# Performance work log

Hardware: AMD Instinct MI355X
Metric: run time of the kernel (lower is better)

The kernel has to match this reference:

```python
import math
import jax, jax.numpy as jnp
import numpy as np

ALPHA = 0.2  # LeakyReLU negative slope
MASK_VAL = -9e15


def _positional_encoding(n: int, d: int) -> jnp.ndarray:
    # Custom PE with a (1 + exp(-pos/100)) decay factor, matching CustomPositionalEncoding
    position = jnp.arange(n, dtype=jnp.float32)[:, None]            # [N,1]
    div_term = jnp.exp(jnp.arange(0, d, 2, dtype=jnp.float32) * (-math.log(10000.0) / d))
    decay = 1.0 + jnp.exp(-position / 100.0)                         # [N,1]
    pe = jnp.zeros((n, d), dtype=jnp.float32)
    pe = pe.at[:, 0::2].set(jnp.sin(position * div_term) * decay)
    pe = pe.at[:, 1::2].set(jnp.cos(position * div_term) * decay)
    return pe[None]                                                  # [1,N,d]


def setup_inputs() -> dict:
    key = jax.random.key(0)
    k_h, k_adj, k_W, k_a = jax.random.split(key, 4)
    B, N, IN_F, OUT_F = 8, 2048, 128, 128
    h = jax.random.normal(k_h, (B, N, IN_F), dtype=jnp.float32)
    # sparse-ish 0/1 adjacency (float, as in the torch module)
    adj = jax.random.randint(k_adj, (B, N, N), 0, 2).astype(jnp.float32)
    # xavier_uniform init scale
    limW = math.sqrt(6.0 / (IN_F + OUT_F))
    W = jax.random.uniform(k_W, (IN_F, OUT_F), minval=-limW, maxval=limW, dtype=jnp.float32)
    lima = math.sqrt(6.0 / (2 * OUT_F + 1))
    a = jax.random.uniform(k_a, (2 * OUT_F, 1), minval=-lima, maxval=lima, dtype=jnp.float32)
    return {"h": h, "adj": adj, "W": W, "a": a}


def reference(h, adj, W, a):
    B, N, _ = h.shape
    out_f = W.shape[1]
    h = h + _positional_encoding(N, h.shape[2])
    # force self-loops
    eye = jnp.eye(N, dtype=adj.dtype)[None]
    adj = jnp.where(eye > 0, jnp.ones_like(adj), adj)
    Wh = jnp.einsum('bni,io->bno', h, W)                 # [B,N,out_f]
    a1 = a[:out_f, 0]
    a2 = a[out_f:, 0]
    s1 = Wh @ a1                                          # [B,N]
    s2 = Wh @ a2                                          # [B,N]
    e = s1[:, :, None] + s2[:, None, :]                   # [B,N,N] additive score
    e = jnp.where(e >= 0, e, ALPHA * e)                   # leaky relu
    attn = jnp.where(adj > 0, e, MASK_VAL)
    attn = jax.nn.softmax(attn, axis=-1)
    # dropout is identity in eval mode
    h_prime = jnp.einsum('bnm,bmo->bno', attn, Wh)        # [B,N,out_f]
    deg = adj.sum(-1)                                     # [B,N]
    valid = deg > 0
    valid = valid.at[:, 0].set(False)
    denom = jnp.clip(valid.sum(1, keepdims=True), 1, None).astype(h_prime.dtype)  # [B,1]
    g = (h_prime * valid[:, :, None]).sum(1) / denom      # [B,out_f] masked mean pool
    return jax.nn.elu(g)
```

## Files before the change

kernel.cpp:

```cpp
#include <hip/hip_runtime.h>
#include <math.h>

#define NN 2048
#define BATCH 8
#define FDIM 128
#define MASKV -9000000000000000.0f
#define LALPHA 0.2f

__global__ void k_zero(float* __restrict__ c, float* __restrict__ gpre) {
    int i = blockIdx.x * 256 + threadIdx.x;
    if (i < BATCH * NN) c[i] = 0.f;
    if (i < BATCH * FDIM) gpre[i] = 0.f;
}

__global__ void k_pe(float* __restrict__ pe) {
    int i = blockIdx.x * 256 + threadIdx.x;
    int n = i >> 7;
    int k = i & 127;
    int jj = k >> 1;
    float dt = expf((float)(2 * jj) * (-0.07195578415606394f));
    float ang = (float)n * dt;
    float decay = 1.f + expf(-(float)n * 0.01f);
    float v = ((k & 1) == 0 ? sinf(ang) : cosf(ang)) * decay;
    pe[i] = v;
}

__global__ __launch_bounds__(256) void k_wh(const float* __restrict__ h,
                                            const float* __restrict__ pe,
                                            const float* __restrict__ W,
                                            const float* __restrict__ a,
                                            float* __restrict__ Wh,
                                            float* __restrict__ s1,
                                            float* __restrict__ s2) {
    __shared__ float w_lds[64 * 128];
    __shared__ float hpe_lds[64 * 68];
    const int b  = blockIdx.y;
    const int n0 = blockIdx.x * 64;
    const int t  = threadIdx.x;
    const int tc = t & 15;
    const int tr = t >> 4;

    float acc[4][8];
#pragma unroll
    for (int i = 0; i < 4; i++)
#pragma unroll
        for (int j = 0; j < 8; j++) acc[i][j] = 0.f;

    for (int kp = 0; kp < 2; ++kp) {
        {
            const float4* wsrc = (const float4*)(W + kp * 64 * 128);
            float4* wdst = (float4*)w_lds;
#pragma unroll
            for (int q = 0; q < 8; q++) wdst[t + q * 256] = wsrc[t + q * 256];
        }
        {
#pragma unroll
            for (int q = 0; q < 4; q++) {
                int f = t + q * 256;
                int r = f >> 4;
                int k4 = (f & 15) << 2;
                int n = n0 + r;
                int kk = kp * 64 + k4;
                const float* hp_src = h + ((size_t)b * NN + n) * FDIM + kk;
                float4 hv = *(const float4*)hp_src;
                float4 pv = *(const float4*)(pe + (size_t)n * FDIM + kk);
                float4 hpv = make_float4(hv.x + pv.x, hv.y + pv.y,
                                         hv.z + pv.z, hv.w + pv.w);
                *(float4*)(hpe_lds + r * 68 + k4) = hpv;
            }
        }
        __syncthreads();
#pragma unroll 4
        for (int k = 0; k < 64; k++) {
            float wv[8];
            float4 wa = *(float4*)(w_lds + k * 128 + tc * 8);
            float4 wb = *(float4*)(w_lds + k * 128 + tc * 8 + 4);
            wv[0] = wa.x; wv[1] = wa.y; wv[2] = wa.z; wv[3] = wa.w;
            wv[4] = wb.x; wv[5] = wb.y; wv[6] = wb.z; wv[7] = wb.w;
#pragma unroll
            for (int i = 0; i < 4; i++) {
                float hv = hpe_lds[(tr * 4 + i) * 68 + k];
#pragma unroll
                for (int j = 0; j < 8; j++) acc[i][j] = fmaf(hv, wv[j], acc[i][j]);
            }
        }
        __syncthreads();
    }

    float a1v[8], a2v[8];
#pragma unroll
    for (int j = 0; j < 8; j++) { a1v[j] = a[tc * 8 + j]; a2v[j] = a[FDIM + tc * 8 + j]; }
#pragma unroll
    for (int i = 0; i < 4; i++) {
        int n = n0 + tr * 4 + i;
        float* dst = Wh + ((size_t)b * NN + n) * FDIM + tc * 8;
        *(float4*)dst = make_float4(acc[i][0], acc[i][1], acc[i][2], acc[i][3]);
        *(float4*)(dst + 4) = make_float4(acc[i][4], acc[i][5], acc[i][6], acc[i][7]);
        float p1 = 0.f, p2 = 0.f;
#pragma unroll
        for (int j = 0; j < 8; j++) {
            p1 = fmaf(acc[i][j], a1v[j], p1);
            p2 = fmaf(acc[i][j], a2v[j], p2);
        }
#pragma unroll
        for (int off = 1; off < 16; off <<= 1) {
            p1 += __shfl_xor(p1, off, 64);
            p2 += __shfl_xor(p2, off, 64);
        }
        if (tc == 0) {
            s1[(size_t)b * NN + n] = p1;
            s2[(size_t)b * NN + n] = p2;
        }
    }
}

__global__ __launch_bounds__(256) void k_attn(const float* __restrict__ adj,
                                              const float* __restrict__ s1,
                                              const float* __restrict__ s2,
                                              float* __restrict__ c) {
    const int b = blockIdx.y;
    const int chunk = blockIdx.x;
    const int t = threadIdx.x;
    const int wave = t >> 6;
    const int lane = t & 63;
    __shared__ float c_lds[NN];
    for (int i = t; i < NN; i += 256) c_lds[i] = 0.f;

    const float* s2b = s2 + (size_t)b * NN;
    float s2v[32];
#pragma unroll
    for (int kq = 0; kq < 8; kq++) {
        float4 v = *(const float4*)(s2b + kq * 256 + lane * 4);
        s2v[kq * 4 + 0] = v.x; s2v[kq * 4 + 1] = v.y;
        s2v[kq * 4 + 2] = v.z; s2v[kq * 4 + 3] = v.w;
    }
    float c_acc[32];
#pragma unroll
    for (int j = 0; j < 32; j++) c_acc[j] = 0.f;

    const int nbase = chunk * 32;
    const float* adjb = adj + (size_t)b * NN * NN;
    const float* s1b = s1 + (size_t)b * NN;

    for (int r = wave; r < 32; r += 4) {
        int n = nbase + r;
        if (n == 0) continue;
        float s1n = s1b[n];
        const float* arow = adjb + (size_t)n * NN;
        float val[32];
        float vmax = MASKV;
#pragma unroll
        for (int kq = 0; kq < 8; kq++) {
            float4 av = *(const float4*)(arow + kq * 256 + lane * 4);
            float a4[4] = {av.x, av.y, av.z, av.w};
#pragma unroll
            for (int e = 0; e < 4; e++) {
                int m = kq * 256 + lane * 4 + e;
                float ev = s1n + s2v[kq * 4 + e];
                ev = (ev >= 0.f) ? ev : LALPHA * ev;
                bool conn = (a4[e] > 0.f) || (m == n);
                float v = conn ? ev : MASKV;
                val[kq * 4 + e] = v;
                vmax = fmaxf(vmax, v);
            }
        }
#pragma unroll
        for (int off = 32; off; off >>= 1) vmax = fmaxf(vmax, __shfl_xor(vmax, off, 64));
        float zsum = 0.f;
#pragma unroll
        for (int j = 0; j < 32; j++) {
            float p = __expf(val[j] - vmax);
            val[j] = p;
            zsum += p;
        }
#pragma unroll
        for (int off = 32; off; off >>= 1) zsum += __shfl_xor(zsum, off, 64);
        float rz = 1.f / zsum;
#pragma unroll
        for (int j = 0; j < 32; j++) c_acc[j] = fmaf(val[j], rz, c_acc[j]);
    }

    __syncthreads();
    for (int w = 0; w < 4; w++) {
        if (wave == w) {
#pragma unroll
            for (int kq = 0; kq < 8; kq++)
#pragma unroll
                for (int e = 0; e < 4; e++)
                    c_lds[kq * 256 + lane * 4 + e] += c_acc[kq * 4 + e];
        }
        __syncthreads();
    }
    for (int i = t; i < NN; i += 256)
        atomicAdd(&c[(size_t)b * NN + i], c_lds[i]);
}

__global__ __launch_bounds__(256) void k_gpre(const float* __restrict__ Wh,
                                              const float* __restrict__ c,
                                              float* __restrict__ gpre) {
    const int b = blockIdx.y;
    const int m0 = blockIdx.x * 64;
    const int t = threadIdx.x;
    const int o = t & 127;
    const int mh = t >> 7;
    __shared__ float c_lds[64];
    if (t < 64) c_lds[t] = c[(size_t)b * NN + m0 + t];
    __syncthreads();
    float acc = 0.f;
    const float* whb = Wh + ((size_t)b * NN + m0 + mh * 32) * FDIM;
#pragma unroll 4
    for (int mm = 0; mm < 32; mm++)
        acc = fmaf(c_lds[mh * 32 + mm], whb[mm * FDIM + o], acc);
    atomicAdd(&gpre[b * FDIM + o], acc);
}

__global__ void k_elu(const float* __restrict__ gpre, float* __restrict__ out) {
    int i = blockIdx.x * 256 + threadIdx.x;
    if (i < BATCH * FDIM) {
        float g = gpre[i] * (1.0f / 2047.0f);
        out[i] = g > 0.f ? g : expm1f(g);
    }
}

extern "C" void kernel_launch(void* const* d_in, const int* in_sizes, int n_in,
                              void* d_out, int out_size, void* d_ws, size_t ws_size,
                              hipStream_t stream) {
    (void)in_sizes; (void)n_in; (void)out_size; (void)ws_size;
    const float* h   = (const float*)d_in[0];
    const float* adj = (const float*)d_in[1];
    const float* W   = (const float*)d_in[2];
    const float* a   = (const float*)d_in[3];
    float* out = (float*)d_out;

    char* ws = (char*)d_ws;
    float* Wh   = (float*)ws;
    float* pe   = (float*)(ws + (size_t)BATCH * NN * FDIM * 4);
    float* s1   = pe + (size_t)NN * FDIM;
    float* s2   = s1 + (size_t)BATCH * NN;
    float* c    = s2 + (size_t)BATCH * NN;
    float* gpre = c + (size_t)BATCH * NN;

    hipLaunchKernelGGL(k_zero, dim3(64), dim3(256), 0, stream, c, gpre);
    hipLaunchKernelGGL(k_pe, dim3(NN * FDIM / 256), dim3(256), 0, stream, pe);
    hipLaunchKernelGGL(k_wh, dim3(NN / 64, BATCH), dim3(256), 0, stream,
                       h, pe, W, a, Wh, s1, s2);
    hipLaunchKernelGGL(k_attn, dim3(NN / 32, BATCH), dim3(256), 0, stream,
                       adj, s1, s2, c);
    hipLaunchKernelGGL(k_gpre, dim3(NN / 64, BATCH), dim3(256), 0, stream,
                       Wh, c, gpre);
    hipLaunchKernelGGL(k_elu, dim3(4), dim3(256), 0, stream, gpre, out);
}
```

Baseline: 223.4 us.

## Replace atomic column-sum accumulation with partial buffers and deterministic reductions

The attention kernel now processes 16 rows per block (doubling the grid). Each wave writes its column-sum partial to its own LDS slice, the slices are summed in one pass, and the block writes a per-chunk partial row instead of issuing global atomics. The pooling and ELU kernels then reduce these partial buffers, which removes the zeroing kernel and all atomics. The cost is extra workspace traffic (an 8x128x2048 partial buffer, about 8 MB, read back in the pooling kernel) and a 64-way serial sum in the final kernel.

```diff
diff --git a/kernel.cpp b/kernel.cpp
--- a/kernel.cpp
+++ b/kernel.cpp
@@ -5,13 +5,6 @@
 #define BATCH 8
 #define FDIM 128
 #define MASKV -9000000000000000.0f
-#define LALPHA 0.2f
-
-__global__ void k_zero(float* __restrict__ c, float* __restrict__ gpre) {
-    int i = blockIdx.x * 256 + threadIdx.x;
-    if (i < BATCH * NN) c[i] = 0.f;
-    if (i < BATCH * FDIM) gpre[i] = 0.f;
-}
 
 __global__ void k_pe(float* __restrict__ pe) {
     int i = blockIdx.x * 256 + threadIdx.x;
@@ -117,14 +110,13 @@
 __global__ __launch_bounds__(256) void k_attn(const float* __restrict__ adj,
                                               const float* __restrict__ s1,
                                               const float* __restrict__ s2,
-                                              float* __restrict__ c) {
+                                              float* __restrict__ c_part) {
     const int b = blockIdx.y;
     const int chunk = blockIdx.x;
     const int t = threadIdx.x;
     const int wave = t >> 6;
     const int lane = t & 63;
-    __shared__ float c_lds[NN];
-    for (int i = t; i < NN; i += 256) c_lds[i] = 0.f;
+    __shared__ float c_lds[4][NN];
 
     const float* s2b = s2 + (size_t)b * NN;
     float s2v[32];
@@ -138,12 +130,13 @@
 #pragma unroll
     for (int j = 0; j < 32; j++) c_acc[j] = 0.f;
 
-    const int nbase = chunk * 32;
+    const int nbase = chunk * 16;
     const float* adjb = adj + (size_t)b * NN * NN;
     const float* s1b = s1 + (size_t)b * NN;
 
-    for (int r = wave; r < 32; r += 4) {
-        int n = nbase + r;
+#pragma unroll 1
+    for (int ri = 0; ri < 4; ri++) {
+        int n = nbase + wave * 4 + ri;
         if (n == 0) continue;
         float s1n = s1b[n];
         const float* arow = adjb + (size_t)n * NN;
@@ -156,8 +149,8 @@
 #pragma unroll
             for (int e = 0; e < 4; e++) {
                 int m = kq * 256 + lane * 4 + e;
-                float ev = s1n + s2v[kq * 4 + e];
-                ev = (ev >= 0.f) ? ev : LALPHA * ev;
+                float x = s1n + s2v[kq * 4 + e];
+                float ev = fmaxf(x, 0.2f * x);
                 bool conn = (a4[e] > 0.f) || (m == n);
                 float v = conn ? ev : MASKV;
                 val[kq * 4 + e] = v;
@@ -180,44 +173,67 @@
         for (int j = 0; j < 32; j++) c_acc[j] = fmaf(val[j], rz, c_acc[j]);
     }
 
+#pragma unroll
+    for (int kq = 0; kq < 8; kq++)
+        *(float4*)(&c_lds[wave][kq * 256 + lane * 4]) =
+            make_float4(c_acc[kq * 4 + 0], c_acc[kq * 4 + 1],
+                        c_acc[kq * 4 + 2], c_acc[kq * 4 + 3]);
     __syncthreads();
-    for (int w = 0; w < 4; w++) {
-        if (wave == w) {
-#pragma unroll
-            for (int kq = 0; kq < 8; kq++)
-#pragma unroll
-                for (int e = 0; e < 4; e++)
-                    c_lds[kq * 256 + lane * 4 + e] += c_acc[kq * 4 + e];
-        }
-        __syncthreads();
-    }
-    for (int i = t; i < NN; i += 256)
-        atomicAdd(&c[(size_t)b * NN + i], c_lds[i]);
+    float* dst = c_part + ((size_t)b * 128 + chunk) * NN;
+#pragma unroll
+    for (int q = 0; q < 2; q++) {
+        int idx = t + q * 256;
+        float4 v0 = ((float4*)c_lds[0])[idx];
+        float4 v1 = ((float4*)c_lds[1])[idx];
+        float4 v2 = ((float4*)c_lds[2])[idx];
+        float4 v3 = ((float4*)c_lds[3])[idx];
+        ((float4*)dst)[idx] = make_float4(v0.x + v1.x + v2.x + v3.x,
+                                          v0.y + v1.y + v2.y + v3.y,
+                                          v0.z + v1.z + v2.z + v3.z,
+                                          v0.w + v1.w + v2.w + v3.w);
+    }
 }
 
 __global__ __launch_bounds__(256) void k_gpre(const float* __restrict__ Wh,
-                                              const float* __restrict__ c,
-                                              float* __restrict__ gpre) {
+                                              const float* __restrict__ c_part,
+                                              float* __restrict__ g_part) {
     const int b = blockIdx.y;
-    const int m0 = blockIdx.x * 64;
+    const int mc = blockIdx.x;
+    const int m0 = mc * 64;
     const int t = threadIdx.x;
+    __shared__ float red[256];
+    __shared__ float c_lds[64];
+
+    {
+        const int mi = t & 63;
+        const int w = t >> 6;
+        const float* cp = c_part + (size_t)b * 128 * NN + m0 + mi;
+        float s = 0.f;
+#pragma unroll 8
+        for (int j = 0; j < 32; j++) s += cp[(size_t)(w * 32 + j) * NN];
+        red[w * 64 + mi] = s;
+    }
+    __syncthreads();
+    if (t < 64) c_lds[t] = red[t] + red[t + 64] + red[t + 128] + red[t + 192];
+    __syncthreads();
+
     const int o = t & 127;
     const int mh = t >> 7;
-    __shared__ float c_lds[64];
-    if (t < 64) c_lds[t] = c[(size_t)b * NN + m0 + t];
-    __syncthreads();
     float acc = 0.f;
     const float* whb = Wh + ((size_t)b * NN + m0 + mh * 32) * FDIM;
 #pragma unroll 4
     for (int mm = 0; mm < 32; mm++)
         acc = fmaf(c_lds[mh * 32 + mm], whb[mm * FDIM + o], acc);
-    atomicAdd(&gpre[b * FDIM + o], acc);
-}
-
-__global__ void k_elu(const float* __restrict__ gpre, float* __restrict__ out) {
+    g_part[((size_t)(mc * 2 + mh)) * (BATCH * FDIM) + b * FDIM + o] = acc;
+}
+
+__global__ void k_elu(const float* __restrict__ g_part, float* __restrict__ out) {
     int i = blockIdx.x * 256 + threadIdx.x;
     if (i < BATCH * FDIM) {
-        float g = gpre[i] * (1.0f / 2047.0f);
+        float s = 0.f;
+#pragma unroll 8
+        for (int p = 0; p < 64; p++) s += g_part[p * (BATCH * FDIM) + i];
+        float g = s * (1.0f / 2047.0f);
         out[i] = g > 0.f ? g : expm1f(g);
     }
 }
@@ -233,20 +249,19 @@
     float* out = (float*)d_out;
 
     char* ws = (char*)d_ws;
-    float* Wh   = (float*)ws;
-    float* pe   = (float*)(ws + (size_t)BATCH * NN * FDIM * 4);
-    float* s1   = pe + (size_t)NN * FDIM;
-    float* s2   = s1 + (size_t)BATCH * NN;
-    float* c    = s2 + (size_t)BATCH * NN;
-    float* gpre = c + (size_t)BATCH * NN;
-
-    hipLaunchKernelGGL(k_zero, dim3(64), dim3(256), 0, stream, c, gpre);
+    float* Wh     = (float*)ws;
+    float* pe     = Wh + (size_t)BATCH * NN * FDIM;
+    float* s1     = pe + (size_t)NN * FDIM;
+    float* s2     = s1 + (size_t)BATCH * NN;
+    float* c_part = s2 + (size_t)BATCH * NN;
+    float* g_part = c_part + (size_t)BATCH * 128 * NN;
+
     hipLaunchKernelGGL(k_pe, dim3(NN * FDIM / 256), dim3(256), 0, stream, pe);
     hipLaunchKernelGGL(k_wh, dim3(NN / 64, BATCH), dim3(256), 0, stream,
                        h, pe, W, a, Wh, s1, s2);
-    hipLaunchKernelGGL(k_attn, dim3(NN / 32, BATCH), dim3(256), 0, stream,
-                       adj, s1, s2, c);
+    hipLaunchKernelGGL(k_attn, dim3(NN / 16, BATCH), dim3(256), 0, stream,
+                       adj, s1, s2, c_part);
     hipLaunchKernelGGL(k_gpre, dim3(NN / 64, BATCH), dim3(256), 0, stream,
-                       Wh, c, gpre);
-    hipLaunchKernelGGL(k_elu, dim3(4), dim3(256), 0, stream, gpre, out);
-}
+                       Wh, c_part, g_part);
+    hipLaunchKernelGGL(k_elu, dim3(4), dim3(256), 0, stream, g_part, out);
+}
```

Result: no change. 226.9 us (+1.6%).
